# Optimization experiments

Hardware: AMD Instinct MI355X
Metric: run time of the kernel (lower is better)

The kernel has to match this reference:

```python
import jax, jax.numpy as jnp
import numpy as np

EMBED_DIM = 1024
MODULE_DIM = 128
MODULE_COUNT = 128  # must equal MODULE_DIM for the original matmul to be valid
N_TOKENS = 16384


def setup_inputs() -> dict:
    key = jax.random.key(0)
    ks = jax.random.split(key, 9)
    s_e = 1.0 / np.sqrt(EMBED_DIM)
    s_d = 1.0 / np.sqrt(MODULE_DIM)
    return {
        "h0": jax.random.normal(ks[0], (N_TOKENS, EMBED_DIM), dtype=jnp.float32),
        "we0_w": jax.random.uniform(ks[1], (MODULE_DIM, EMBED_DIM), minval=-s_e, maxval=s_e, dtype=jnp.float32),
        "we0_b": jax.random.uniform(ks[2], (MODULE_DIM,), minval=-s_e, maxval=s_e, dtype=jnp.float32),
        "ws_w": jax.random.uniform(ks[3], (MODULE_COUNT, MODULE_DIM), minval=-s_d, maxval=s_d, dtype=jnp.float32),
        "ws_b": jax.random.uniform(ks[4], (MODULE_COUNT,), minval=-s_d, maxval=s_d, dtype=jnp.float32),
        "wm_w": jax.random.uniform(ks[5], (MODULE_COUNT, MODULE_DIM, MODULE_DIM), minval=-s_d, maxval=s_d, dtype=jnp.float32),
        "wm_b": jax.random.uniform(ks[6], (MODULE_COUNT, MODULE_DIM), minval=-s_d, maxval=s_d, dtype=jnp.float32),
        "we1_w": jax.random.uniform(ks[7], (EMBED_DIM, MODULE_DIM), minval=-s_d, maxval=s_d, dtype=jnp.float32),
        "we1_b": jax.random.uniform(ks[8], (EMBED_DIM,), minval=-s_d, maxval=s_d, dtype=jnp.float32),
    }


def reference(h0, we0_w, we0_b, ws_w, ws_b, wm_w, wm_b, we1_w, we1_b):
    # h0: [N, E]
    enc = h0 @ we0_w.T + we0_b                                   # [N, D]
    # stacked expert linears: acts[m, n, k] = relu(sum_d enc[n,d] * wm_w[m,k,d] + wm_b[m,k])
    acts = jax.nn.relu(jnp.einsum('nd,mkd->mnk', enc, wm_w) + wm_b[:, None, :])  # [M, N, D]
    # gating logits [N, M]; NOTE: softmax over dim 0 (the batch axis), faithful to original
    gate = jax.nn.softmax(enc @ ws_w.T + ws_b, axis=0)           # [N, M]
    # original: matmul(acts.transpose(0,1) [N,M,D], gate[...,None] [N,M,1]) with D == M
    # mixed[n, i] = sum_j acts[i, n, j] * gate[n, j]
    mixed = jnp.einsum('inj,nj->ni', acts, gate)                 # [N, M] (== [N, D])
    decoded = mixed @ we1_w.T + we1_b                            # [N, E]
    return jax.nn.relu(decoded + h0)
```

## Files before the change

### kernel.cpp

```cpp
#include <hip/hip_runtime.h>


#define N_TOK   16384
#define EMB     1024
#define MDIM    128

typedef __attribute__((ext_vector_type(8))) short   short8;
typedef __attribute__((ext_vector_type(4))) float   f32x4;
typedef __attribute__((ext_vector_type(4))) float   fv4;
typedef __attribute__((ext_vector_type(4))) unsigned short us4;

static __device__ __forceinline__ unsigned short f2bf(float f) {
    union { float f; unsigned u; } v; v.f = f;
    unsigned r = v.u + 0x7FFFu + ((v.u >> 16) & 1u);
    return (unsigned short)(r >> 16);
}
static __device__ __forceinline__ float bf2f_lo(unsigned u) {
    union { unsigned u; float f; } v; v.u = u << 16; return v.f;
}
static __device__ __forceinline__ float bf2f_hi(unsigned u) {
    union { unsigned u; float f; } v; v.u = u & 0xffff0000u; return v.f;
}

__global__ void k_convert_all(const float* __restrict__ wm_w,
                              const float* __restrict__ we0_w,
                              const float* __restrict__ we1_w,
                              const float* __restrict__ ws_w,
                              unsigned short* __restrict__ dst) {
    const int NFV4 = 593920;
    for (int i = blockIdx.x * blockDim.x + threadIdx.x; i < NFV4;
         i += gridDim.x * blockDim.x) {
        const float* src;
        if (i < 524288)       src = wm_w  + (size_t)i * 4;
        else if (i < 557056)  src = we0_w + (size_t)(i - 524288) * 4;
        else if (i < 589824)  src = we1_w + (size_t)(i - 557056) * 4;
        else                  src = ws_w  + (size_t)(i - 589824) * 4;
        fv4 v = *(const fv4*)src;
        us4 o;
        o.x = f2bf(v.x); o.y = f2bf(v.y); o.z = f2bf(v.z); o.w = f2bf(v.w);
        *(us4*)(dst + (size_t)i * 4) = o;
    }
}


__global__ __launch_bounds__(256) void k_enc(const float* __restrict__ h0,
                                             const unsigned short* __restrict__ we0b,
                                             const unsigned short* __restrict__ wsb,
                                             const float* __restrict__ we0_bias,
                                             const float* __restrict__ ws_bias,
                                             unsigned short* __restrict__ encT,
                                             float* __restrict__ logT) {
    __shared__ unsigned short Wt[128 * 128];
    __shared__ unsigned short Ht[32 * 128];
    __shared__ unsigned short Et[32 * 128];

    const int tid = threadIdx.x;
    const int lane = tid & 63, w = tid >> 6;
    const int c = lane & 15, g = lane >> 4;
    const int wd = w >> 1, wt = w & 1;
    const int t0 = blockIdx.x * 32;

    f32x4 acc[4] = {};
    for (int ks = 0; ks < 8; ++ks) {
        #pragma unroll
        for (int it = 0; it < 8; ++it) {
            int m = it * 256 + tid;
            int row = m >> 4, gc = m & 15;
            short8 v = *(const short8*)(we0b + row * 1024 + ks * 128 + gc * 8);
            *(short8*)&Wt[row * 128 + ((gc ^ (row & 7)) * 8)] = v;
        }
        #pragma unroll
        for (int it = 0; it < 2; ++it) {
            int m = it * 256 + tid;
            int row = m >> 4, gc = m & 15;
            const float* hp = h0 + (size_t)(t0 + row) * 1024 + ks * 128 + gc * 8;
            fv4 v0 = *(const fv4*)hp;
            fv4 v1 = *(const fv4*)(hp + 4);
            short8 ov;
            ov[0] = (short)f2bf(v0.x); ov[1] = (short)f2bf(v0.y);
            ov[2] = (short)f2bf(v0.z); ov[3] = (short)f2bf(v0.w);
            ov[4] = (short)f2bf(v1.x); ov[5] = (short)f2bf(v1.y);
            ov[6] = (short)f2bf(v1.z); ov[7] = (short)f2bf(v1.w);
            *(short8*)&Ht[row * 128 + ((gc ^ (row & 7)) * 8)] = ov;
        }
        __syncthreads();
        #pragma unroll
        for (int s = 0; s < 4; ++s) {
            int gk = s * 4 + g;
            int brow = wt * 16 + c;
            short8 b = *(const short8*)&Ht[brow * 128 + ((gk ^ (brow & 7)) * 8)];
            #pragma unroll
            for (int jf = 0; jf < 4; ++jf) {
                int j = wd * 64 + jf * 16 + c;
                short8 a = *(const short8*)&Wt[j * 128 + ((gk ^ (j & 7)) * 8)];
                acc[jf] = __builtin_amdgcn_mfma_f32_16x16x32_bf16(a, b, acc[jf], 0, 0, 0);
            }
        }
        __syncthreads();
    }
    const int tile = blockIdx.x * 2 + wt;
    const int erow = wt * 16 + c;
    #pragma unroll
    for (int f = 0; f < 4; ++f) {
        int d0 = wd * 64 + f * 16 + 4 * g;
        int s = wd * 2 + (f >> 1);
        int chunk = ((f & 1) ? 2 : 0) + (g >> 1);
        int e = (g & 1) * 4;
        fv4 bi = *(const fv4*)(we0_bias + d0);
        us4 o;
        o.x = f2bf(acc[f][0] + bi.x);
        o.y = f2bf(acc[f][1] + bi.y);
        o.z = f2bf(acc[f][2] + bi.z);
        o.w = f2bf(acc[f][3] + bi.w);
        *(us4*)(encT + (size_t)tile * 2048 + s * 512 + (chunk * 16 + c) * 8 + e) = o;
        int cg = d0 >> 3, off = d0 & 7;
        *(us4*)&Et[erow * 128 + ((cg ^ (erow & 7)) * 8) + off] = o;
    }
    __syncthreads();

    short8 al[4][4];
    #pragma unroll
    for (int jf = 0; jf < 4; ++jf)
        #pragma unroll
        for (int s = 0; s < 4; ++s)
            al[jf][s] = *(const short8*)(wsb + (wd * 64 + jf * 16 + c) * 128 + s * 32 + g * 8);
    short8 bl[4];
    #pragma unroll
    for (int s = 0; s < 4; ++s) {
        int cg2 = s * 4 + g;
        bl[s] = *(const short8*)&Et[erow * 128 + ((cg2 ^ (erow & 7)) * 8)];
    }
    f32x4 acc2[4] = {};
    #pragma unroll
    for (int s = 0; s < 4; ++s)
        #pragma unroll
        for (int jf = 0; jf < 4; ++jf)
            acc2[jf] = __builtin_amdgcn_mfma_f32_16x16x32_bf16(al[jf][s], bl[s], acc2[jf], 0, 0, 0);
    const int tokc = t0 + wt * 16 + c;
    #pragma unroll
    for (int jf = 0; jf < 4; ++jf) {
        int m0 = wd * 64 + jf * 16 + 4 * g;
        fv4 bs = *(const fv4*)(ws_bias + m0);
        logT[(size_t)(m0 + 0) * N_TOK + tokc] = acc2[jf][0] + bs.x;
        logT[(size_t)(m0 + 1) * N_TOK + tokc] = acc2[jf][1] + bs.y;
        logT[(size_t)(m0 + 2) * N_TOK + tokc] = acc2[jf][2] + bs.z;
        logT[(size_t)(m0 + 3) * N_TOK + tokc] = acc2[jf][3] + bs.w;
    }
}

__global__ __launch_bounds__(256) void k_softmax0(const float* __restrict__ logT,
                                                  unsigned short* __restrict__ gateT) {
    __shared__ float red[8];
    const int m = blockIdx.x;
    const int tid = threadIdx.x;
    const int lane = tid & 63, wv = tid >> 6;
    const float* row = logT + (size_t)m * N_TOK;

    fv4 v[16];
    float vmax = -3.0e38f;
    #pragma unroll
    for (int it = 0; it < 16; ++it) {
        v[it] = *(const fv4*)(row + it * 1024 + tid * 4);
        vmax = fmaxf(vmax, fmaxf(fmaxf(v[it].x, v[it].y), fmaxf(v[it].z, v[it].w)));
    }
    #pragma unroll
    for (int o = 32; o > 0; o >>= 1) vmax = fmaxf(vmax, __shfl_xor(vmax, o));
    if (lane == 0) red[wv] = vmax;
    __syncthreads();
    const float bmax = fmaxf(fmaxf(red[0], red[1]), fmaxf(red[2], red[3]));

    float s = 0.f;
    #pragma unroll
    for (int it = 0; it < 16; ++it) {
        v[it].x = __expf(v[it].x - bmax); v[it].y = __expf(v[it].y - bmax);
        v[it].z = __expf(v[it].z - bmax); v[it].w = __expf(v[it].w - bmax);
        s += v[it].x + v[it].y + v[it].z + v[it].w;
    }
    #pragma unroll
    for (int o = 32; o > 0; o >>= 1) s += __shfl_xor(s, o);
    if (lane == 0) red[4 + wv] = s;
    __syncthreads();
    const float inv = 1.f / (red[4] + red[5] + red[6] + red[7]);

    const int q  = m >> 5;
    const int w8 = ((m >> 4) & 1) * 4 + (m & 3);
    const int gl = ((m & 15) >> 2) * 16;
    #pragma unroll
    for (int it = 0; it < 16; ++it) {
        int t = it * 1024 + tid * 4;
        float pv[4] = { v[it].x * inv, v[it].y * inv, v[it].z * inv, v[it].w * inv };
        #pragma unroll
        for (int k = 0; k < 4; ++k) {
            int tok = t + k;
            gateT[(size_t)(tok >> 4) * 2048 + q * 512 + (gl + (tok & 15)) * 8 + w8] = f2bf(pv[k]);
        }
    }
}

__global__ __launch_bounds__(256)
__attribute__((amdgpu_waves_per_eu(2, 2)))
void k_mix(const unsigned short* __restrict__ wmb,
           const unsigned short* __restrict__ encT,
           const unsigned short* __restrict__ gateT,
           const float* __restrict__ wm_bias,
           unsigned short* __restrict__ mixT) {
    const int bid = blockIdx.x;
    const int tg = bid & 3, i = bid >> 2;
    const int tid = threadIdx.x;
    const int lane = tid & 63, w = tid >> 6;
    const int c = lane & 15, g = lane >> 4;

    const unsigned short* wmi = wmb + (size_t)i * 16384;
    short8 a[8][4];
    #pragma unroll
    for (int jf = 0; jf < 8; ++jf)
        #pragma unroll
        for (int s = 0; s < 4; ++s) {
            a[jf][s] = *(const short8*)(wmi + (jf * 16 + c) * 128 + s * 32 + g * 8);
            asm volatile("" : "+v"(a[jf][s]));
        }
    f32x4 bias4[8];
    #pragma unroll
    for (int f = 0; f < 8; ++f)
        bias4[f] = *(const f32x4*)(wm_bias + i * 128 + f * 16 + 4 * g);

    const int si = i >> 5, ch = (i & 31) >> 3, ei = i & 7;

    #pragma unroll 1
    for (int rr = 0; rr < 64; ++rr) {
        const int tile = tg * 256 + rr * 4 + w;
        const unsigned short* ep = encT + (size_t)tile * 2048 + lane * 8;
        short8 b0 = *(const short8*)(ep);
        short8 b1 = *(const short8*)(ep + 512);
        short8 b2 = *(const short8*)(ep + 1024);
        short8 b3 = *(const short8*)(ep + 1536);
        const unsigned* gp = (const unsigned*)(gateT + (size_t)tile * 2048) + lane * 4;
        uint4 G0 = *(const uint4*)(gp);
        uint4 G1 = *(const uint4*)(gp + 256);
        uint4 G2 = *(const uint4*)(gp + 512);
        uint4 G3 = *(const uint4*)(gp + 768);

        f32x4 acc[8];
        #pragma unroll
        for (int jf = 0; jf < 8; ++jf)
            acc[jf] = __builtin_amdgcn_mfma_f32_16x16x32_bf16(a[jf][0], b0, bias4[jf], 0, 0, 0);
        #pragma unroll
        for (int jf = 0; jf < 8; ++jf)
            acc[jf] = __builtin_amdgcn_mfma_f32_16x16x32_bf16(a[jf][1], b1, acc[jf], 0, 0, 0);
        #pragma unroll
        for (int jf = 0; jf < 8; ++jf)
            acc[jf] = __builtin_amdgcn_mfma_f32_16x16x32_bf16(a[jf][2], b2, acc[jf], 0, 0, 0);
        #pragma unroll
        for (int jf = 0; jf < 8; ++jf)
            acc[jf] = __builtin_amdgcn_mfma_f32_16x16x32_bf16(a[jf][3], b3, acc[jf], 0, 0, 0);

        float p0 = 0.f, p1 = 0.f, p2 = 0.f, p3 = 0.f;
        #define EPI(F, GA, GB) {                                        \
            p0 += fmaxf(acc[F][0], 0.f) * bf2f_lo(GA);                  \
            p1 += fmaxf(acc[F][1], 0.f) * bf2f_hi(GA);                  \
            p2 += fmaxf(acc[F][2], 0.f) * bf2f_lo(GB);                  \
            p3 += fmaxf(acc[F][3], 0.f) * bf2f_hi(GB);                  \
        }
        EPI(0, G0.x, G0.y) EPI(1, G0.z, G0.w)
        EPI(2, G1.x, G1.y) EPI(3, G1.z, G1.w)
        EPI(4, G2.x, G2.y) EPI(5, G2.z, G2.w)
        EPI(6, G3.x, G3.y) EPI(7, G3.z, G3.w)
        #undef EPI
        float p = (p0 + p1) + (p2 + p3);
        p += __shfl_xor(p, 16);
        p += __shfl_xor(p, 32);
        if (lane < 16)
            mixT[(size_t)tile * 2048 + si * 512 + (ch * 16 + lane) * 8 + ei] = f2bf(p);
    }
}

__global__ __launch_bounds__(256)
__attribute__((amdgpu_waves_per_eu(2, 2)))
void k_dec(const unsigned short* __restrict__ we1b,
           const unsigned short* __restrict__ mixT,
           const float* __restrict__ we1_bias,
           const float* __restrict__ h0,
           float* __restrict__ out) {
    const int bid = blockIdx.x;
    const int eb = bid & 7, tg = bid >> 3;
    const int e0 = eb * 128;
    const int tid = threadIdx.x;
    const int lane = tid & 63, w = tid >> 6;
    const int c = lane & 15, g = lane >> 4;

    short8 a[8][4];
    #pragma unroll
    for (int jf = 0; jf < 8; ++jf)
        #pragma unroll
        for (int s = 0; s < 4; ++s) {
            a[jf][s] = *(const short8*)(we1b + (size_t)(e0 + jf * 16 + c) * 128 + s * 32 + g * 8);
            asm volatile("" : "+v"(a[jf][s]));
        }
    fv4 bi[8];
    #pragma unroll
    for (int f = 0; f < 8; ++f)
        bi[f] = *(const fv4*)(we1_bias + e0 + f * 16 + 4 * g);

    #pragma unroll 1
    for (int t = 0; t < 4; ++t) {
        const int tokr = tg * 256 + t * 64 + w * 16 + c;
        const int tile = tg * 16 + t * 4 + w;
        fv4 h[8];
        #pragma unroll
        for (int f = 0; f < 8; ++f)
            h[f] = *(const fv4*)(h0 + (size_t)tokr * 1024 + e0 + f * 16 + 4 * g);
        const unsigned short* mp = mixT + (size_t)tile * 2048 + lane * 8;
        short8 b[4];
        #pragma unroll
        for (int s = 0; s < 4; ++s)
            b[s] = *(const short8*)(mp + s * 512);

        f32x4 acc[8] = {};
        #pragma unroll
        for (int s = 0; s < 4; ++s)
            #pragma unroll
            for (int jf = 0; jf < 8; ++jf)
                acc[jf] = __builtin_amdgcn_mfma_f32_16x16x32_bf16(a[jf][s], b[s], acc[jf], 0, 0, 0);

        #pragma unroll
        for (int f = 0; f < 8; ++f) {
            fv4 o;
            o.x = fmaxf(acc[f][0] + bi[f].x + h[f].x, 0.f);
            o.y = fmaxf(acc[f][1] + bi[f].y + h[f].y, 0.f);
            o.z = fmaxf(acc[f][2] + bi[f].z + h[f].z, 0.f);
            o.w = fmaxf(acc[f][3] + bi[f].w + h[f].w, 0.f);
            *(fv4*)(out + (size_t)tokr * 1024 + e0 + f * 16 + 4 * g) = o;
        }
    }
}

extern "C" void kernel_launch(void* const* d_in, const int* in_sizes, int n_in,
                              void* d_out, int out_size, void* d_ws, size_t ws_size,
                              hipStream_t stream) {
    const float* h0    = (const float*)d_in[0];
    const float* we0_w = (const float*)d_in[1];
    const float* we0_b = (const float*)d_in[2];
    const float* ws_w  = (const float*)d_in[3];
    const float* ws_b  = (const float*)d_in[4];
    const float* wm_w  = (const float*)d_in[5];
    const float* wm_b  = (const float*)d_in[6];
    const float* we1_w = (const float*)d_in[7];
    const float* we1_b = (const float*)d_in[8];
    float* out = (float*)d_out;

    unsigned short* wmb   = (unsigned short*)d_ws;
    unsigned short* we0b  = wmb  + 2097152;
    unsigned short* we1b  = we0b + 131072;
    unsigned short* wsb   = we1b + 131072;
    unsigned short* encT  = wsb  + 16384;
    float*          logT  = (float*)(encT + 2097152);
    unsigned short* gateT = (unsigned short*)(logT + 2097152);
    unsigned short* mixT  = gateT + 2097152;

    k_convert_all<<<640, 256, 0, stream>>>(wm_w, we0_w, we1_w, ws_w, wmb);
    k_enc<<<512, 256, 0, stream>>>(h0, we0b, wsb, we0_b, ws_b, encT, logT);
    k_softmax0<<<128, 256, 0, stream>>>(logT, gateT);
    k_mix<<<512, 256, 0, stream>>>(wmb, encT, gateT, wm_b, mixT);
    k_dec<<<512, 256, 0, stream>>>(we1b, mixT, we1_b, h0, out);
}
```

Measured before the change: 173.9 us.

## Software-pipeline k_mix operand loads and widen softmax blocks to 1024 threads

k_mix now prefetches the next tile's enc and gate operands while the current tile's MFMAs and epilogue run. It uses double-buffered gate registers and s_setprio around the MFMA blocks, so load latency is hidden behind compute instead of being exposed at the top of each iteration. Separately, k_softmax0 runs 1024 threads per row instead of 256, with 4 vectors per thread, to increase memory parallelism for its 128 blocks. The pipelining raises register pressure in a kernel already pinned to 2 waves per EU, and the final iteration does a redundant reload.

```diff
diff --git a/kernel.cpp b/kernel.cpp
--- a/kernel.cpp
+++ b/kernel.cpp
@@ -148,46 +148,51 @@
     }
 }
 
-__global__ __launch_bounds__(256) void k_softmax0(const float* __restrict__ logT,
-                                                  unsigned short* __restrict__ gateT) {
-    __shared__ float red[8];
+__global__ __launch_bounds__(1024) void k_softmax0(const float* __restrict__ logT,
+                                                   unsigned short* __restrict__ gateT) {
+    __shared__ float red[32];
     const int m = blockIdx.x;
     const int tid = threadIdx.x;
     const int lane = tid & 63, wv = tid >> 6;
     const float* row = logT + (size_t)m * N_TOK;
 
-    fv4 v[16];
+    fv4 v[4];
     float vmax = -3.0e38f;
     #pragma unroll
-    for (int it = 0; it < 16; ++it) {
-        v[it] = *(const fv4*)(row + it * 1024 + tid * 4);
+    for (int it = 0; it < 4; ++it) {
+        v[it] = *(const fv4*)(row + it * 4096 + tid * 4);
         vmax = fmaxf(vmax, fmaxf(fmaxf(v[it].x, v[it].y), fmaxf(v[it].z, v[it].w)));
     }
     #pragma unroll
     for (int o = 32; o > 0; o >>= 1) vmax = fmaxf(vmax, __shfl_xor(vmax, o));
     if (lane == 0) red[wv] = vmax;
     __syncthreads();
-    const float bmax = fmaxf(fmaxf(red[0], red[1]), fmaxf(red[2], red[3]));
+    float bmax = -3.0e38f;
+    #pragma unroll
+    for (int k = 0; k < 16; ++k) bmax = fmaxf(bmax, red[k]);
 
     float s = 0.f;
     #pragma unroll
-    for (int it = 0; it < 16; ++it) {
+    for (int it = 0; it < 4; ++it) {
         v[it].x = __expf(v[it].x - bmax); v[it].y = __expf(v[it].y - bmax);
         v[it].z = __expf(v[it].z - bmax); v[it].w = __expf(v[it].w - bmax);
         s += v[it].x + v[it].y + v[it].z + v[it].w;
     }
     #pragma unroll
     for (int o = 32; o > 0; o >>= 1) s += __shfl_xor(s, o);
-    if (lane == 0) red[4 + wv] = s;
+    if (lane == 0) red[16 + wv] = s;
     __syncthreads();
-    const float inv = 1.f / (red[4] + red[5] + red[6] + red[7]);
+    float bs = 0.f;
+    #pragma unroll
+    for (int k = 0; k < 16; ++k) bs += red[16 + k];
+    const float inv = 1.f / bs;
 
     const int q  = m >> 5;
     const int w8 = ((m >> 4) & 1) * 4 + (m & 3);
     const int gl = ((m & 15) >> 2) * 16;
     #pragma unroll
-    for (int it = 0; it < 16; ++it) {
-        int t = it * 1024 + tid * 4;
+    for (int it = 0; it < 4; ++it) {
+        int t = it * 4096 + tid * 4;
         float pv[4] = { v[it].x * inv, v[it].y * inv, v[it].z * inv, v[it].w * inv };
         #pragma unroll
         for (int k = 0; k < 4; ++k) {
@@ -225,53 +230,107 @@
         bias4[f] = *(const f32x4*)(wm_bias + i * 128 + f * 16 + 4 * g);
 
     const int si = i >> 5, ch = (i & 31) >> 3, ei = i & 7;
+    const size_t base = (size_t)(tg * 256 + w) * 2048 + lane * 8;
+    const unsigned short* encP  = encT + base;
+    const unsigned* gateP = (const unsigned*)(gateT + (size_t)(tg * 256 + w) * 2048) + lane * 4;
+    unsigned short* mixP = mixT + (size_t)(tg * 256 + w) * 2048 + si * 512 + (ch * 16 + lane) * 8 + ei;
+
+    short8 b0 = *(const short8*)(encP);
+    short8 b1 = *(const short8*)(encP + 512);
+    short8 b2 = *(const short8*)(encP + 1024);
+    short8 b3 = *(const short8*)(encP + 1536);
+    uint4 GA0 = *(const uint4*)(gateP);
+    uint4 GA1 = *(const uint4*)(gateP + 256);
+    uint4 GA2 = *(const uint4*)(gateP + 512);
+    uint4 GA3 = *(const uint4*)(gateP + 768);
+    uint4 GB0, GB1, GB2, GB3;
+
+    #define MFMA_BLOCK(NOFF) {                                                      \
+        const unsigned short* epn = encP + (size_t)(NOFF) * 2048;                   \
+        __builtin_amdgcn_s_setprio(1);                                              \
+        _Pragma("unroll")                                                           \
+        for (int jf = 0; jf < 8; ++jf)                                              \
+            acc[jf] = __builtin_amdgcn_mfma_f32_16x16x32_bf16(a[jf][0], b0, bias4[jf], 0, 0, 0); \
+        b0 = *(const short8*)(epn);                                                 \
+        _Pragma("unroll")                                                           \
+        for (int jf = 0; jf < 8; ++jf)                                              \
+            acc[jf] = __builtin_amdgcn_mfma_f32_16x16x32_bf16(a[jf][1], b1, acc[jf], 0, 0, 0); \
+        b1 = *(const short8*)(epn + 512);                                           \
+        _Pragma("unroll")                                                           \
+        for (int jf = 0; jf < 8; ++jf)                                              \
+            acc[jf] = __builtin_amdgcn_mfma_f32_16x16x32_bf16(a[jf][2], b2, acc[jf], 0, 0, 0); \
+        b2 = *(const short8*)(epn + 1024);                                          \
+        _Pragma("unroll")                                                           \
+        for (int jf = 0; jf < 8; ++jf)                                              \
+            acc[jf] = __builtin_amdgcn_mfma_f32_16x16x32_bf16(a[jf][3], b3, acc[jf], 0, 0, 0); \
+        b3 = *(const short8*)(epn + 1536);                                          \
+        __builtin_amdgcn_s_setprio(0);                                              \
+    }
+    #define EPI_ALL(GX0, GX1, GX2, GX3, TOFF) {                                     \
+        float p0 = 0.f, p1 = 0.f, p2 = 0.f, p3 = 0.f;                               \
+        p0 += fmaxf(acc[0][0], 0.f) * bf2f_lo(GX0.x);                               \
+        p1 += fmaxf(acc[0][1], 0.f) * bf2f_hi(GX0.x);                               \
+        p2 += fmaxf(acc[0][2], 0.f) * bf2f_lo(GX0.y);                               \
+        p3 += fmaxf(acc[0][3], 0.f) * bf2f_hi(GX0.y);                               \
+        p0 += fmaxf(acc[1][0], 0.f) * bf2f_lo(GX0.z);                               \
+        p1 += fmaxf(acc[1][1], 0.f) * bf2f_hi(GX0.z);                               \
+        p2 += fmaxf(acc[1][2], 0.f) * bf2f_lo(GX0.w);                               \
+        p3 += fmaxf(acc[1][3], 0.f) * bf2f_hi(GX0.w);                               \
+        p0 += fmaxf(acc[2][0], 0.f) * bf2f_lo(GX1.x);                               \
+        p1 += fmaxf(acc[2][1], 0.f) * bf2f_hi(GX1.x);                               \
+        p2 += fmaxf(acc[2][2], 0.f) * bf2f_lo(GX1.y);                               \
+        p3 += fmaxf(acc[2][3], 0.f) * bf2f_hi(GX1.y);                               \
+        p0 += fmaxf(acc[3][0], 0.f) * bf2f_lo(GX1.z);                               \
+        p1 += fmaxf(acc[3][1], 0.f) * bf2f_hi(GX1.z);                               \
+        p2 += fmaxf(acc[3][2], 0.f) * bf2f_lo(GX1.w);                               \
+        p3 += fmaxf(acc[3][3], 0.f) * bf2f_hi(GX1.w);                               \
+        p0 += fmaxf(acc[4][0], 0.f) * bf2f_lo(GX2.x);                               \
+        p1 += fmaxf(acc[4][1], 0.f) * bf2f_hi(GX2.x);                               \
+        p2 += fmaxf(acc[4][2], 0.f) * bf2f_lo(GX2.y);                               \
+        p3 += fmaxf(acc[4][3], 0.f) * bf2f_hi(GX2.y);                               \
+        p0 += fmaxf(acc[5][0], 0.f) * bf2f_lo(GX2.z);                               \
+        p1 += fmaxf(acc[5][1], 0.f) * bf2f_hi(GX2.z);                               \
+        p2 += fmaxf(acc[5][2], 0.f) * bf2f_lo(GX2.w);                               \
+        p3 += fmaxf(acc[5][3], 0.f) * bf2f_hi(GX2.w);                               \
+        p0 += fmaxf(acc[6][0], 0.f) * bf2f_lo(GX3.x);                               \
+        p1 += fmaxf(acc[6][1], 0.f) * bf2f_hi(GX3.x);                               \
+        p2 += fmaxf(acc[6][2], 0.f) * bf2f_lo(GX3.y);                               \
+        p3 += fmaxf(acc[6][3], 0.f) * bf2f_hi(GX3.y);                               \
+        p0 += fmaxf(acc[7][0], 0.f) * bf2f_lo(GX3.z);                               \
+        p1 += fmaxf(acc[7][1], 0.f) * bf2f_hi(GX3.z);                               \
+        p2 += fmaxf(acc[7][2], 0.f) * bf2f_lo(GX3.w);                               \
+        p3 += fmaxf(acc[7][3], 0.f) * bf2f_hi(GX3.w);                               \
+        float p = (p0 + p1) + (p2 + p3);                                            \
+        p += __shfl_xor(p, 16);                                                     \
+        p += __shfl_xor(p, 32);                                                     \
+        if (lane < 16) *(mixP + (size_t)(TOFF) * 2048) = f2bf(p);                   \
+    }
 
     #pragma unroll 1
-    for (int rr = 0; rr < 64; ++rr) {
-        const int tile = tg * 256 + rr * 4 + w;
-        const unsigned short* ep = encT + (size_t)tile * 2048 + lane * 8;
-        short8 b0 = *(const short8*)(ep);
-        short8 b1 = *(const short8*)(ep + 512);
-        short8 b2 = *(const short8*)(ep + 1024);
-        short8 b3 = *(const short8*)(ep + 1536);
-        const unsigned* gp = (const unsigned*)(gateT + (size_t)tile * 2048) + lane * 4;
-        uint4 G0 = *(const uint4*)(gp);
-        uint4 G1 = *(const uint4*)(gp + 256);
-        uint4 G2 = *(const uint4*)(gp + 512);
-        uint4 G3 = *(const uint4*)(gp + 768);
-
+    for (int rr = 0; rr < 64; rr += 2) {
         f32x4 acc[8];
-        #pragma unroll
-        for (int jf = 0; jf < 8; ++jf)
-            acc[jf] = __builtin_amdgcn_mfma_f32_16x16x32_bf16(a[jf][0], b0, bias4[jf], 0, 0, 0);
-        #pragma unroll
-        for (int jf = 0; jf < 8; ++jf)
-            acc[jf] = __builtin_amdgcn_mfma_f32_16x16x32_bf16(a[jf][1], b1, acc[jf], 0, 0, 0);
-        #pragma unroll
-        for (int jf = 0; jf < 8; ++jf)
-            acc[jf] = __builtin_amdgcn_mfma_f32_16x16x32_bf16(a[jf][2], b2, acc[jf], 0, 0, 0);
-        #pragma unroll
-        for (int jf = 0; jf < 8; ++jf)
-            acc[jf] = __builtin_amdgcn_mfma_f32_16x16x32_bf16(a[jf][3], b3, acc[jf], 0, 0, 0);
-
-        float p0 = 0.f, p1 = 0.f, p2 = 0.f, p3 = 0.f;
-        #define EPI(F, GA, GB) {                                        \
-            p0 += fmaxf(acc[F][0], 0.f) * bf2f_lo(GA);                  \
-            p1 += fmaxf(acc[F][1], 0.f) * bf2f_hi(GA);                  \
-            p2 += fmaxf(acc[F][2], 0.f) * bf2f_lo(GB);                  \
-            p3 += fmaxf(acc[F][3], 0.f) * bf2f_hi(GB);                  \
-        }
-        EPI(0, G0.x, G0.y) EPI(1, G0.z, G0.w)
-        EPI(2, G1.x, G1.y) EPI(3, G1.z, G1.w)
-        EPI(4, G2.x, G2.y) EPI(5, G2.z, G2.w)
-        EPI(6, G3.x, G3.y) EPI(7, G3.z, G3.w)
-        #undef EPI
-        float p = (p0 + p1) + (p2 + p3);
-        p += __shfl_xor(p, 16);
-        p += __shfl_xor(p, 32);
-        if (lane < 16)
-            mixT[(size_t)tile * 2048 + si * 512 + (ch * 16 + lane) * 8 + ei] = f2bf(p);
-    }
+        MFMA_BLOCK(4 * (rr + 1));
+        {
+            const unsigned* gpn = gateP + (size_t)(4 * (rr + 1)) * 512;
+            GB0 = *(const uint4*)(gpn);
+            GB1 = *(const uint4*)(gpn + 256);
+            GB2 = *(const uint4*)(gpn + 512);
+            GB3 = *(const uint4*)(gpn + 768);
+        }
+        EPI_ALL(GA0, GA1, GA2, GA3, 4 * rr);
+        const int nn = (rr < 62) ? rr + 2 : 62;
+        MFMA_BLOCK(4 * nn);
+        {
+            const unsigned* gpn = gateP + (size_t)(4 * nn) * 512;
+            GA0 = *(const uint4*)(gpn);
+            GA1 = *(const uint4*)(gpn + 256);
+            GA2 = *(const uint4*)(gpn + 512);
+            GA3 = *(const uint4*)(gpn + 768);
+        }
+        EPI_ALL(GB0, GB1, GB2, GB3, 4 * (rr + 1));
+    }
+    #undef MFMA_BLOCK
+    #undef EPI_ALL
 }
 
 __global__ __launch_bounds__(256)
@@ -359,7 +418,7 @@
 
     k_convert_all<<<640, 256, 0, stream>>>(wm_w, we0_w, we1_w, ws_w, wmb);
     k_enc<<<512, 256, 0, stream>>>(h0, we0b, wsb, we0_b, ws_b, encT, logT);
-    k_softmax0<<<128, 256, 0, stream>>>(logT, gateT);
+    k_softmax0<<<128, 1024, 0, stream>>>(logT, gateT);
     k_mix<<<512, 256, 0, stream>>>(wmb, encT, gateT, wm_b, mixT);
     k_dec<<<512, 256, 0, stream>>>(we1b, mixT, we1_b, h0, out);
 }
```

New measurement: 171.7 us. No clear change (-1.2%).

## Share enc/gate tiles across experts in k_mix via double-buffered LDS; fp32 gates

Applied to the files above, without the earlier changes.

k_mix now gives each wave of a block its own expert, and all four waves share one token tile. That tile is staged through double-buffered LDS with a register prefetch of the next tile, which cuts the global reads of enc and gate per expert by four. Gates are stored in fp32 in a layout the epilogue reads directly, so the bf16 unpacking goes away. The softmax uses 1024-thread blocks, and mixT reuses the logT buffer. The costs are a per-tile __syncthreads, doubled gate bytes, and extra LDS traffic.

```diff
diff --git a/kernel.cpp b/kernel.cpp
--- a/kernel.cpp
+++ b/kernel.cpp
@@ -14,12 +14,6 @@
     union { float f; unsigned u; } v; v.f = f;
     unsigned r = v.u + 0x7FFFu + ((v.u >> 16) & 1u);
     return (unsigned short)(r >> 16);
-}
-static __device__ __forceinline__ float bf2f_lo(unsigned u) {
-    union { unsigned u; float f; } v; v.u = u << 16; return v.f;
-}
-static __device__ __forceinline__ float bf2f_hi(unsigned u) {
-    union { unsigned u; float f; } v; v.u = u & 0xffff0000u; return v.f;
 }
 
 __global__ void k_convert_all(const float* __restrict__ wm_w,
@@ -148,51 +142,54 @@
     }
 }
 
-__global__ __launch_bounds__(256) void k_softmax0(const float* __restrict__ logT,
-                                                  unsigned short* __restrict__ gateT) {
-    __shared__ float red[8];
+__global__ __launch_bounds__(1024) void k_softmax0(const float* __restrict__ logT,
+                                                   float* __restrict__ gateF) {
+    __shared__ float red[32];
     const int m = blockIdx.x;
     const int tid = threadIdx.x;
     const int lane = tid & 63, wv = tid >> 6;
     const float* row = logT + (size_t)m * N_TOK;
 
-    fv4 v[16];
+    fv4 v[4];
     float vmax = -3.0e38f;
     #pragma unroll
-    for (int it = 0; it < 16; ++it) {
-        v[it] = *(const fv4*)(row + it * 1024 + tid * 4);
+    for (int it = 0; it < 4; ++it) {
+        v[it] = *(const fv4*)(row + it * 4096 + tid * 4);
         vmax = fmaxf(vmax, fmaxf(fmaxf(v[it].x, v[it].y), fmaxf(v[it].z, v[it].w)));
     }
     #pragma unroll
     for (int o = 32; o > 0; o >>= 1) vmax = fmaxf(vmax, __shfl_xor(vmax, o));
     if (lane == 0) red[wv] = vmax;
     __syncthreads();
-    const float bmax = fmaxf(fmaxf(red[0], red[1]), fmaxf(red[2], red[3]));
+    float bmax = -3.0e38f;
+    #pragma unroll
+    for (int k = 0; k < 16; ++k) bmax = fmaxf(bmax, red[k]);
 
     float s = 0.f;
     #pragma unroll
-    for (int it = 0; it < 16; ++it) {
+    for (int it = 0; it < 4; ++it) {
         v[it].x = __expf(v[it].x - bmax); v[it].y = __expf(v[it].y - bmax);
         v[it].z = __expf(v[it].z - bmax); v[it].w = __expf(v[it].w - bmax);
         s += v[it].x + v[it].y + v[it].z + v[it].w;
     }
     #pragma unroll
     for (int o = 32; o > 0; o >>= 1) s += __shfl_xor(s, o);
-    if (lane == 0) red[4 + wv] = s;
+    if (lane == 0) red[16 + wv] = s;
     __syncthreads();
-    const float inv = 1.f / (red[4] + red[5] + red[6] + red[7]);
-
-    const int q  = m >> 5;
-    const int w8 = ((m >> 4) & 1) * 4 + (m & 3);
-    const int gl = ((m & 15) >> 2) * 16;
-    #pragma unroll
-    for (int it = 0; it < 16; ++it) {
-        int t = it * 1024 + tid * 4;
+    float bs = 0.f;
+    #pragma unroll
+    for (int k = 0; k < 16; ++k) bs += red[16 + k];
+    const float inv = 1.f / bs;
+
+    const int mbase = ((m >> 4) << 8) + (((m & 15) >> 2) << 6) + (m & 3);
+    #pragma unroll
+    for (int it = 0; it < 4; ++it) {
+        int t = it * 4096 + tid * 4;
         float pv[4] = { v[it].x * inv, v[it].y * inv, v[it].z * inv, v[it].w * inv };
         #pragma unroll
         for (int k = 0; k < 4; ++k) {
             int tok = t + k;
-            gateT[(size_t)(tok >> 4) * 2048 + q * 512 + (gl + (tok & 15)) * 8 + w8] = f2bf(pv[k]);
+            gateF[(size_t)(tok >> 4) * 2048 + mbase + (tok & 15) * 4] = pv[k];
         }
     }
 }
@@ -201,14 +198,18 @@
 __attribute__((amdgpu_waves_per_eu(2, 2)))
 void k_mix(const unsigned short* __restrict__ wmb,
            const unsigned short* __restrict__ encT,
-           const unsigned short* __restrict__ gateT,
+           const float* __restrict__ gateF,
            const float* __restrict__ wm_bias,
            unsigned short* __restrict__ mixT) {
+    __shared__ unsigned short ebuf[2][2048];
+    __shared__ float gbuf[2][2048];
+
     const int bid = blockIdx.x;
-    const int tg = bid & 3, i = bid >> 2;
+    const int ig = bid >> 4, tg = bid & 15;
     const int tid = threadIdx.x;
     const int lane = tid & 63, w = tid >> 6;
     const int c = lane & 15, g = lane >> 4;
+    const int i = ig * 4 + w;
 
     const unsigned short* wmi = wmb + (size_t)i * 16384;
     short8 a[8][4];
@@ -225,21 +226,36 @@
         bias4[f] = *(const f32x4*)(wm_bias + i * 128 + f * 16 + 4 * g);
 
     const int si = i >> 5, ch = (i & 31) >> 3, ei = i & 7;
+    const int tile0 = tg * 64;
+    unsigned short* mixP = mixT + (size_t)tile0 * 2048 + si * 512 + (ch * 16 + lane) * 8 + ei;
+
+    {
+        uint4 eg = *(const uint4*)(encT + (size_t)tile0 * 2048 + tid * 8);
+        uint4 g0 = *(const uint4*)(gateF + (size_t)tile0 * 2048 + tid * 4);
+        uint4 g1 = *(const uint4*)(gateF + (size_t)tile0 * 2048 + 1024 + tid * 4);
+        *(uint4*)&ebuf[0][tid * 8] = eg;
+        *(uint4*)&gbuf[0][tid * 4] = g0;
+        *(uint4*)&gbuf[0][1024 + tid * 4] = g1;
+    }
+    __syncthreads();
 
     #pragma unroll 1
-    for (int rr = 0; rr < 64; ++rr) {
-        const int tile = tg * 256 + rr * 4 + w;
-        const unsigned short* ep = encT + (size_t)tile * 2048 + lane * 8;
-        short8 b0 = *(const short8*)(ep);
-        short8 b1 = *(const short8*)(ep + 512);
-        short8 b2 = *(const short8*)(ep + 1024);
-        short8 b3 = *(const short8*)(ep + 1536);
-        const unsigned* gp = (const unsigned*)(gateT + (size_t)tile * 2048) + lane * 4;
-        uint4 G0 = *(const uint4*)(gp);
-        uint4 G1 = *(const uint4*)(gp + 256);
-        uint4 G2 = *(const uint4*)(gp + 512);
-        uint4 G3 = *(const uint4*)(gp + 768);
-
+    for (int t = 0; t < 64; ++t) {
+        const int cur = t & 1;
+        uint4 eg = {}, g0 = {}, g1 = {};
+        if (t < 63) {
+            const size_t nt = (size_t)(tile0 + t + 1) * 2048;
+            eg = *(const uint4*)(encT + nt + tid * 8);
+            g0 = *(const uint4*)(gateF + nt + tid * 4);
+            g1 = *(const uint4*)(gateF + nt + 1024 + tid * 4);
+        }
+
+        short8 b0 = *(const short8*)&ebuf[cur][lane * 8];
+        short8 b1 = *(const short8*)&ebuf[cur][512 + lane * 8];
+        short8 b2 = *(const short8*)&ebuf[cur][1024 + lane * 8];
+        short8 b3 = *(const short8*)&ebuf[cur][1536 + lane * 8];
+
+        __builtin_amdgcn_s_setprio(1);
         f32x4 acc[8];
         #pragma unroll
         for (int jf = 0; jf < 8; ++jf)
@@ -253,24 +269,28 @@
         #pragma unroll
         for (int jf = 0; jf < 8; ++jf)
             acc[jf] = __builtin_amdgcn_mfma_f32_16x16x32_bf16(a[jf][3], b3, acc[jf], 0, 0, 0);
+        __builtin_amdgcn_s_setprio(0);
 
         float p0 = 0.f, p1 = 0.f, p2 = 0.f, p3 = 0.f;
-        #define EPI(F, GA, GB) {                                        \
-            p0 += fmaxf(acc[F][0], 0.f) * bf2f_lo(GA);                  \
-            p1 += fmaxf(acc[F][1], 0.f) * bf2f_hi(GA);                  \
-            p2 += fmaxf(acc[F][2], 0.f) * bf2f_lo(GB);                  \
-            p3 += fmaxf(acc[F][3], 0.f) * bf2f_hi(GB);                  \
-        }
-        EPI(0, G0.x, G0.y) EPI(1, G0.z, G0.w)
-        EPI(2, G1.x, G1.y) EPI(3, G1.z, G1.w)
-        EPI(4, G2.x, G2.y) EPI(5, G2.z, G2.w)
-        EPI(6, G3.x, G3.y) EPI(7, G3.z, G3.w)
-        #undef EPI
+        #pragma unroll
+        for (int f = 0; f < 8; ++f) {
+            fv4 G = *(const fv4*)&gbuf[cur][f * 256 + lane * 4];
+            p0 += fmaxf(acc[f][0], 0.f) * G.x;
+            p1 += fmaxf(acc[f][1], 0.f) * G.y;
+            p2 += fmaxf(acc[f][2], 0.f) * G.z;
+            p3 += fmaxf(acc[f][3], 0.f) * G.w;
+        }
         float p = (p0 + p1) + (p2 + p3);
         p += __shfl_xor(p, 16);
         p += __shfl_xor(p, 32);
-        if (lane < 16)
-            mixT[(size_t)tile * 2048 + si * 512 + (ch * 16 + lane) * 8 + ei] = f2bf(p);
+        if (lane < 16) *(mixP + (size_t)t * 2048) = f2bf(p);
+
+        if (t < 63) {
+            *(uint4*)&ebuf[cur ^ 1][tid * 8] = eg;
+            *(uint4*)&gbuf[cur ^ 1][tid * 4] = g0;
+            *(uint4*)&gbuf[cur ^ 1][1024 + tid * 4] = g1;
+        }
+        __syncthreads();
     }
 }
 
@@ -354,12 +374,12 @@
     unsigned short* wsb   = we1b + 131072;
     unsigned short* encT  = wsb  + 16384;
     float*          logT  = (float*)(encT + 2097152);
-    unsigned short* gateT = (unsigned short*)(logT + 2097152);
-    unsigned short* mixT  = gateT + 2097152;
+    float*          gateF = logT + 2097152;
+    unsigned short* mixT  = (unsigned short*)logT;
 
     k_convert_all<<<640, 256, 0, stream>>>(wm_w, we0_w, we1_w, ws_w, wmb);
     k_enc<<<512, 256, 0, stream>>>(h0, we0b, wsb, we0_b, ws_b, encT, logT);
-    k_softmax0<<<128, 256, 0, stream>>>(logT, gateT);
-    k_mix<<<512, 256, 0, stream>>>(wmb, encT, gateT, wm_b, mixT);
+    k_softmax0<<<128, 1024, 0, stream>>>(logT, gateF);
+    k_mix<<<512, 256, 0, stream>>>(wmb, encT, gateF, wm_b, mixT);
     k_dec<<<512, 256, 0, stream>>>(we1b, mixT, we1_b, h0, out);
 }
```

After: 171.5 us. Within noise of the previous version (-1.4%).

## Software-pipeline k_mix global loads with inline asm and widen softmax blocks

Applied to the files above, without the earlier changes.

Restructures the k_mix token loop into a double-buffered pipeline. Inline-asm global loads prefetch the enc tile two steps ahead and the gate tile one step ahead, and explicit vmcnt waits gate their use. Dummy loads pad the counter sequence, and setprio raises priority around the MFMA bursts, so memory latency should overlap with matrix math. The softmax kernel separately moves to 1024-thread blocks, giving each thread fewer elements and more parallelism per expert row. The hand-counted vmcnt scheme is fragile and adds redundant loads.

```diff
diff --git a/kernel.cpp b/kernel.cpp
--- a/kernel.cpp
+++ b/kernel.cpp
@@ -148,46 +148,51 @@
     }
 }
 
-__global__ __launch_bounds__(256) void k_softmax0(const float* __restrict__ logT,
-                                                  unsigned short* __restrict__ gateT) {
-    __shared__ float red[8];
+__global__ __launch_bounds__(1024) void k_softmax0(const float* __restrict__ logT,
+                                                   unsigned short* __restrict__ gateT) {
+    __shared__ float red[32];
     const int m = blockIdx.x;
     const int tid = threadIdx.x;
     const int lane = tid & 63, wv = tid >> 6;
     const float* row = logT + (size_t)m * N_TOK;
 
-    fv4 v[16];
+    fv4 v[4];
     float vmax = -3.0e38f;
     #pragma unroll
-    for (int it = 0; it < 16; ++it) {
-        v[it] = *(const fv4*)(row + it * 1024 + tid * 4);
+    for (int it = 0; it < 4; ++it) {
+        v[it] = *(const fv4*)(row + it * 4096 + tid * 4);
         vmax = fmaxf(vmax, fmaxf(fmaxf(v[it].x, v[it].y), fmaxf(v[it].z, v[it].w)));
     }
     #pragma unroll
     for (int o = 32; o > 0; o >>= 1) vmax = fmaxf(vmax, __shfl_xor(vmax, o));
     if (lane == 0) red[wv] = vmax;
     __syncthreads();
-    const float bmax = fmaxf(fmaxf(red[0], red[1]), fmaxf(red[2], red[3]));
+    float bmax = -3.0e38f;
+    #pragma unroll
+    for (int k = 0; k < 16; ++k) bmax = fmaxf(bmax, red[k]);
 
     float s = 0.f;
     #pragma unroll
-    for (int it = 0; it < 16; ++it) {
+    for (int it = 0; it < 4; ++it) {
         v[it].x = __expf(v[it].x - bmax); v[it].y = __expf(v[it].y - bmax);
         v[it].z = __expf(v[it].z - bmax); v[it].w = __expf(v[it].w - bmax);
         s += v[it].x + v[it].y + v[it].z + v[it].w;
     }
     #pragma unroll
     for (int o = 32; o > 0; o >>= 1) s += __shfl_xor(s, o);
-    if (lane == 0) red[4 + wv] = s;
+    if (lane == 0) red[16 + wv] = s;
     __syncthreads();
-    const float inv = 1.f / (red[4] + red[5] + red[6] + red[7]);
+    float bs = 0.f;
+    #pragma unroll
+    for (int k = 0; k < 16; ++k) bs += red[16 + k];
+    const float inv = 1.f / bs;
 
     const int q  = m >> 5;
     const int w8 = ((m >> 4) & 1) * 4 + (m & 3);
     const int gl = ((m & 15) >> 2) * 16;
     #pragma unroll
-    for (int it = 0; it < 16; ++it) {
-        int t = it * 1024 + tid * 4;
+    for (int it = 0; it < 4; ++it) {
+        int t = it * 4096 + tid * 4;
         float pv[4] = { v[it].x * inv, v[it].y * inv, v[it].z * inv, v[it].w * inv };
         #pragma unroll
         for (int k = 0; k < 4; ++k) {
@@ -196,6 +201,12 @@
         }
     }
 }
+
+#define GLOAD(dst, base, imm)                                           \
+    asm volatile("global_load_dwordx4 %0, %1, off offset:" imm          \
+                 : "=v"(dst) : "v"(base))
+#define VMW(n) do { asm volatile("s_waitcnt vmcnt(" n ")" ::: "memory");\
+                    __builtin_amdgcn_sched_barrier(0); } while (0)
 
 __global__ __launch_bounds__(256)
 __attribute__((amdgpu_waves_per_eu(2, 2)))
@@ -221,57 +232,116 @@
         }
     f32x4 bias4[8];
     #pragma unroll
-    for (int f = 0; f < 8; ++f)
+    for (int f = 0; f < 8; ++f) {
         bias4[f] = *(const f32x4*)(wm_bias + i * 128 + f * 16 + 4 * g);
+        asm volatile("" : "+v"(bias4[f]));
+    }
 
     const int si = i >> 5, ch = (i & 31) >> 3, ei = i & 7;
+    const char* encB  = (const char*)(encT  + (size_t)(tg * 256 + w) * 2048) + lane * 16;
+    const char* gateB = (const char*)(gateT + (size_t)(tg * 256 + w) * 2048) + lane * 16;
+    unsigned short* mixB = mixT + (size_t)(tg * 256 + w) * 2048 + si * 512 + (ch * 16 + lane) * 8 + ei;
+
+    uint4 bA0, bA1, bA2, bA3, bB0, bB1, bB2, bB3, g0, g1, g2, g3, dmy;
+    GLOAD(bA0, encB, "0"); GLOAD(bA1, encB, "1024");
+    GLOAD(bA2, encB, "2048"); GLOAD(bA3, encB, "3072");
+    { const char* e1 = encB + 16384;
+      GLOAD(bB0, e1, "0"); GLOAD(bB1, e1, "1024");
+      GLOAD(bB2, e1, "2048"); GLOAD(bB3, e1, "3072"); }
+    GLOAD(dmy, encB, "0"); GLOAD(dmy, encB, "0"); GLOAD(dmy, encB, "0");
+    GLOAD(dmy, encB, "0"); GLOAD(dmy, encB, "0"); GLOAD(dmy, encB, "0");
+    GLOAD(g0, gateB, "0"); GLOAD(g1, gateB, "1024");
+    GLOAD(g2, gateB, "2048"); GLOAD(g3, gateB, "3072");
+
+    #define AS8(x) __builtin_bit_cast(short8, x)
+    #define MFMAB(B0, B1, B2, B3)                                              \
+        {                                                                      \
+            short8 vb0 = AS8(B0), vb1 = AS8(B1), vb2 = AS8(B2), vb3 = AS8(B3); \
+            __builtin_amdgcn_s_setprio(1);                                     \
+            _Pragma("unroll")                                                  \
+            for (int jf = 0; jf < 8; ++jf)                                     \
+                acc[jf] = __builtin_amdgcn_mfma_f32_16x16x32_bf16(a[jf][0], vb0, bias4[jf], 0, 0, 0); \
+            _Pragma("unroll")                                                  \
+            for (int jf = 0; jf < 8; ++jf)                                     \
+                acc[jf] = __builtin_amdgcn_mfma_f32_16x16x32_bf16(a[jf][1], vb1, acc[jf], 0, 0, 0); \
+            _Pragma("unroll")                                                  \
+            for (int jf = 0; jf < 8; ++jf)                                     \
+                acc[jf] = __builtin_amdgcn_mfma_f32_16x16x32_bf16(a[jf][2], vb2, acc[jf], 0, 0, 0); \
+            _Pragma("unroll")                                                  \
+            for (int jf = 0; jf < 8; ++jf)                                     \
+                acc[jf] = __builtin_amdgcn_mfma_f32_16x16x32_bf16(a[jf][3], vb3, acc[jf], 0, 0, 0); \
+            __builtin_amdgcn_s_setprio(0);                                     \
+        }
+    #define EPI_ST(TT)                                                         \
+        {                                                                      \
+            float p0 = 0.f, p1 = 0.f, p2 = 0.f, p3 = 0.f;                      \
+            p0 += fmaxf(acc[0][0], 0.f) * bf2f_lo(g0.x);                       \
+            p1 += fmaxf(acc[0][1], 0.f) * bf2f_hi(g0.x);                       \
+            p2 += fmaxf(acc[0][2], 0.f) * bf2f_lo(g0.y);                       \
+            p3 += fmaxf(acc[0][3], 0.f) * bf2f_hi(g0.y);                       \
+            p0 += fmaxf(acc[1][0], 0.f) * bf2f_lo(g0.z);                       \
+            p1 += fmaxf(acc[1][1], 0.f) * bf2f_hi(g0.z);                       \
+            p2 += fmaxf(acc[1][2], 0.f) * bf2f_lo(g0.w);                       \
+            p3 += fmaxf(acc[1][3], 0.f) * bf2f_hi(g0.w);                       \
+            p0 += fmaxf(acc[2][0], 0.f) * bf2f_lo(g1.x);                       \
+            p1 += fmaxf(acc[2][1], 0.f) * bf2f_hi(g1.x);                       \
+            p2 += fmaxf(acc[2][2], 0.f) * bf2f_lo(g1.y);                       \
+            p3 += fmaxf(acc[2][3], 0.f) * bf2f_hi(g1.y);                       \
+            p0 += fmaxf(acc[3][0], 0.f) * bf2f_lo(g1.z);                       \
+            p1 += fmaxf(acc[3][1], 0.f) * bf2f_hi(g1.z);                       \
+            p2 += fmaxf(acc[3][2], 0.f) * bf2f_lo(g1.w);                       \
+            p3 += fmaxf(acc[3][3], 0.f) * bf2f_hi(g1.w);                       \
+            p0 += fmaxf(acc[4][0], 0.f) * bf2f_lo(g2.x);                       \
+            p1 += fmaxf(acc[4][1], 0.f) * bf2f_hi(g2.x);                       \
+            p2 += fmaxf(acc[4][2], 0.f) * bf2f_lo(g2.y);                       \
+            p3 += fmaxf(acc[4][3], 0.f) * bf2f_hi(g2.y);                       \
+            p0 += fmaxf(acc[5][0], 0.f) * bf2f_lo(g2.z);                       \
+            p1 += fmaxf(acc[5][1], 0.f) * bf2f_hi(g2.z);                       \
+            p2 += fmaxf(acc[5][2], 0.f) * bf2f_lo(g2.w);                       \
+            p3 += fmaxf(acc[5][3], 0.f) * bf2f_hi(g2.w);                       \
+            p0 += fmaxf(acc[6][0], 0.f) * bf2f_lo(g3.x);                       \
+            p1 += fmaxf(acc[6][1], 0.f) * bf2f_hi(g3.x);                       \
+            p2 += fmaxf(acc[6][2], 0.f) * bf2f_lo(g3.y);                       \
+            p3 += fmaxf(acc[6][3], 0.f) * bf2f_hi(g3.y);                       \
+            p0 += fmaxf(acc[7][0], 0.f) * bf2f_lo(g3.z);                       \
+            p1 += fmaxf(acc[7][1], 0.f) * bf2f_hi(g3.z);                       \
+            p2 += fmaxf(acc[7][2], 0.f) * bf2f_lo(g3.w);                       \
+            p3 += fmaxf(acc[7][3], 0.f) * bf2f_hi(g3.w);                       \
+            float p = (p0 + p1) + (p2 + p3);                                   \
+            p += __shfl_xor(p, 16);                                            \
+            p += __shfl_xor(p, 32);                                            \
+            unsigned pv = f2bf(p);                                             \
+            if (lane < 16)                                                     \
+                asm volatile("global_store_short %0, %1, off"                  \
+                             :: "v"(mixB + (size_t)(TT) * 8192), "v"(pv)       \
+                             : "memory");                                      \
+        }
+    #define HALF(TT, B0, B1, B2, B3)                                           \
+        {                                                                      \
+            VMW("14");                                                         \
+            f32x4 acc[8];                                                      \
+            MFMAB(B0, B1, B2, B3);                                             \
+            { int tb = (TT) + 2 < 64 ? (TT) + 2 : 63;                          \
+              const char* eb = encB + (size_t)tb * 16384;                      \
+              GLOAD(B0, eb, "0"); GLOAD(B1, eb, "1024");                       \
+              GLOAD(B2, eb, "2048"); GLOAD(B3, eb, "3072"); }                  \
+            VMW("4");                                                          \
+            EPI_ST(TT);                                                        \
+            { int tn = (TT) + 1 < 64 ? (TT) + 1 : 63;                          \
+              const char* gb = gateB + (size_t)tn * 16384;                     \
+              GLOAD(g0, gb, "0"); GLOAD(g1, gb, "1024");                       \
+              GLOAD(g2, gb, "2048"); GLOAD(g3, gb, "3072"); }                  \
+        }
 
     #pragma unroll 1
-    for (int rr = 0; rr < 64; ++rr) {
-        const int tile = tg * 256 + rr * 4 + w;
-        const unsigned short* ep = encT + (size_t)tile * 2048 + lane * 8;
-        short8 b0 = *(const short8*)(ep);
-        short8 b1 = *(const short8*)(ep + 512);
-        short8 b2 = *(const short8*)(ep + 1024);
-        short8 b3 = *(const short8*)(ep + 1536);
-        const unsigned* gp = (const unsigned*)(gateT + (size_t)tile * 2048) + lane * 4;
-        uint4 G0 = *(const uint4*)(gp);
-        uint4 G1 = *(const uint4*)(gp + 256);
-        uint4 G2 = *(const uint4*)(gp + 512);
-        uint4 G3 = *(const uint4*)(gp + 768);
-
-        f32x4 acc[8];
-        #pragma unroll
-        for (int jf = 0; jf < 8; ++jf)
-            acc[jf] = __builtin_amdgcn_mfma_f32_16x16x32_bf16(a[jf][0], b0, bias4[jf], 0, 0, 0);
-        #pragma unroll
-        for (int jf = 0; jf < 8; ++jf)
-            acc[jf] = __builtin_amdgcn_mfma_f32_16x16x32_bf16(a[jf][1], b1, acc[jf], 0, 0, 0);
-        #pragma unroll
-        for (int jf = 0; jf < 8; ++jf)
-            acc[jf] = __builtin_amdgcn_mfma_f32_16x16x32_bf16(a[jf][2], b2, acc[jf], 0, 0, 0);
-        #pragma unroll
-        for (int jf = 0; jf < 8; ++jf)
-            acc[jf] = __builtin_amdgcn_mfma_f32_16x16x32_bf16(a[jf][3], b3, acc[jf], 0, 0, 0);
-
-        float p0 = 0.f, p1 = 0.f, p2 = 0.f, p3 = 0.f;
-        #define EPI(F, GA, GB) {                                        \
-            p0 += fmaxf(acc[F][0], 0.f) * bf2f_lo(GA);                  \
-            p1 += fmaxf(acc[F][1], 0.f) * bf2f_hi(GA);                  \
-            p2 += fmaxf(acc[F][2], 0.f) * bf2f_lo(GB);                  \
-            p3 += fmaxf(acc[F][3], 0.f) * bf2f_hi(GB);                  \
-        }
-        EPI(0, G0.x, G0.y) EPI(1, G0.z, G0.w)
-        EPI(2, G1.x, G1.y) EPI(3, G1.z, G1.w)
-        EPI(4, G2.x, G2.y) EPI(5, G2.z, G2.w)
-        EPI(6, G3.x, G3.y) EPI(7, G3.z, G3.w)
-        #undef EPI
-        float p = (p0 + p1) + (p2 + p3);
-        p += __shfl_xor(p, 16);
-        p += __shfl_xor(p, 32);
-        if (lane < 16)
-            mixT[(size_t)tile * 2048 + si * 512 + (ch * 16 + lane) * 8 + ei] = f2bf(p);
-    }
+    for (int t = 0; t < 64; t += 2) {
+        HALF(t,     bA0, bA1, bA2, bA3);
+        HALF(t + 1, bB0, bB1, bB2, bB3);
+    }
+    #undef HALF
+    #undef EPI_ST
+    #undef MFMAB
+    #undef AS8
 }
 
 __global__ __launch_bounds__(256)
@@ -359,7 +429,7 @@
 
     k_convert_all<<<640, 256, 0, stream>>>(wm_w, we0_w, we1_w, ws_w, wmb);
     k_enc<<<512, 256, 0, stream>>>(h0, we0b, wsb, we0_b, ws_b, encT, logT);
-    k_softmax0<<<128, 256, 0, stream>>>(logT, gateT);
+    k_softmax0<<<128, 1024, 0, stream>>>(logT, gateT);
     k_mix<<<512, 256, 0, stream>>>(wmb, encT, gateT, wm_b, mixT);
     k_dec<<<512, 256, 0, stream>>>(we1b, mixT, we1_b, h0, out);
 }
```

Result: faster. 168.6 us (-3.0%).
